# Kernel tuning notes

Hardware: AMD Instinct MI355X
Metric: run time of the kernel (lower is better)

## Reference

```python
import jax, jax.numpy as jnp
import numpy as np

N, E = 100000, 1600000
IN_C, H, C = 256, 4, 64
NEG_SLOPE = 0.2


def setup_inputs() -> dict:
    key = jax.random.key(0)
    k1, k2, k3, k4, k5 = jax.random.split(key, 5)
    x = jax.random.normal(k1, (N, IN_C), dtype=jnp.float32)
    edge_index = jax.random.randint(k2, (2, E), 0, N, dtype=jnp.int64)
    # GATConv params: lin weight [IN_C, H*C], attention vectors [H, C], bias [C] (concat=False)
    W = jax.random.normal(k3, (IN_C, H * C), dtype=jnp.float32) / np.sqrt(IN_C)
    att_src = jax.random.normal(k4, (H, C), dtype=jnp.float32) / np.sqrt(C)
    att_dst = jax.random.normal(k5, (H, C), dtype=jnp.float32) / np.sqrt(C)
    bias = jnp.zeros((C,), dtype=jnp.float32)
    return {"x": x, "edge_index": edge_index, "W": W,
            "att_src": att_src, "att_dst": att_dst, "bias": bias}


def reference(x, edge_index, W, att_src, att_dst, bias):
    n = x.shape[0]
    # GATConv adds self-loops by default
    loops = jnp.arange(n, dtype=edge_index.dtype)
    src = jnp.concatenate([edge_index[0], loops])  # message source j
    dst = jnp.concatenate([edge_index[1], loops])  # message target i

    h = (x @ W).reshape(n, H, C)                       # [N,H,C]
    a_src = jnp.einsum('nhc,hc->nh', h, att_src)       # [N,H]
    a_dst = jnp.einsum('nhc,hc->nh', h, att_dst)       # [N,H]

    e = jax.nn.leaky_relu(a_src[src] + a_dst[dst], NEG_SLOPE)  # [E+N,H]
    m = jax.ops.segment_max(e, dst, num_segments=n)            # per-target max
    e = jnp.exp(e - m[dst])
    denom = jax.ops.segment_sum(e, dst, num_segments=n)
    alpha = e / (denom[dst] + 1e-16)                           # softmax over incoming edges

    out = jax.ops.segment_sum(alpha[:, :, None] * h[src], dst, num_segments=n)  # [N,H,C]
    return out.mean(axis=1) + bias  # concat=False -> mean over heads, [N,C]
```

## Files before the change

kernel.cpp:

```cpp
#include <hip/hip_runtime.h>

#define N_NODES 100000
#define N_EDGES 1600000
#define TOT (N_EDGES + N_NODES)
#define IN_CH 256
#define NHEAD 4
#define CH 64
#define HC 256
#define NEG_SLOPE 0.2f
#define CAP 48
#define NGEMM ((N_NODES + 63) / 64)
#define DOTS_BLOCKS ((N_NODES + 3) / 4)
#define SCT_BLOCKS ((TOT + 255) / 256)

typedef _Float16 half8 __attribute__((ext_vector_type(8)));
typedef _Float16 h2v __attribute__((ext_vector_type(2)));
typedef float f32x4 __attribute__((ext_vector_type(4)));
typedef unsigned short ushort_t;
typedef unsigned int uint_t;

static __device__ __forceinline__ ushort_t f2h(float f) {
  _Float16 h = (_Float16)f;
  return __builtin_bit_cast(ushort_t, h);
}

static __device__ __forceinline__ void gload_lds16(const char* g, char* l) {
  __builtin_amdgcn_global_load_lds(
      (const __attribute__((address_space(1))) unsigned int*)g,
      (__attribute__((address_space(3))) unsigned int*)l, 16, 0, 0);
}

__global__ __launch_bounds__(256) void conv_w(const float* __restrict__ W,
                                              const float* __restrict__ att_src,
                                              const float* __restrict__ att_dst,
                                              uint4* __restrict__ Wt_arr,
                                              float4* __restrict__ Was4,
                                              float4* __restrict__ Wad4,
                                              int* __restrict__ cursor) {
  int id = blockIdx.x * 256 + threadIdx.x;
  if (blockIdx.x == 32) {
    int k = threadIdx.x;
    float s[4] = {}, d[4] = {};
#pragma unroll
    for (int h = 0; h < 4; ++h) {
      const float4* wr = reinterpret_cast<const float4*>(W + (size_t)k * HC + h * 64);
      const float4* asr = reinterpret_cast<const float4*>(att_src + h * 64);
      const float4* adr = reinterpret_cast<const float4*>(att_dst + h * 64);
      for (int c4 = 0; c4 < 16; ++c4) {
        float4 w = wr[c4], a = asr[c4], b = adr[c4];
        s[h] += w.x * a.x + w.y * a.y + w.z * a.z + w.w * a.w;
        d[h] += w.x * b.x + w.y * b.y + w.z * b.z + w.w * b.w;
      }
    }
    Was4[k] = make_float4(s[0], s[1], s[2], s[3]);
    Wad4[k] = make_float4(d[0], d[1], d[2], d[3]);
  } else {
    int lane = id & 63;
    int n = (id >> 6) & 15;
    int ks = id >> 10;
    int col = n * 16 + (lane & 15);
    int kbase = ks * 32 + (lane >> 4) * 8;
    ushort_t h[8];
#pragma unroll
    for (int j = 0; j < 8; ++j) h[j] = f2h(W[(size_t)(kbase + j) * HC + col]);
    uint4 u;
    u.x = (uint_t)h[0] | ((uint_t)h[1] << 16);
    u.y = (uint_t)h[2] | ((uint_t)h[3] << 16);
    u.z = (uint_t)h[4] | ((uint_t)h[5] << 16);
    u.w = (uint_t)h[6] | ((uint_t)h[7] << 16);
    Wt_arr[id] = u;
  }
  for (int i = id; i < N_NODES / 4; i += 33 * 256)
    reinterpret_cast<int4*>(cursor)[i] = make_int4(0, 0, 0, 0);
}

__global__ __launch_bounds__(256) void dots(const float* __restrict__ X,
                                            const float4* __restrict__ Was4,
                                            const float4* __restrict__ Wad4,
                                            float* __restrict__ as_buf,
                                            float* __restrict__ ad_buf) {
  int n = blockIdx.x * 4 + (threadIdx.x >> 6);
  int lane = threadIdx.x & 63;
  if (n >= N_NODES) return;
  float4 xv = reinterpret_cast<const float4*>(X)[(size_t)n * 64 + lane];
  const float4* ws = Was4 + lane * 4;
  const float4* wd = Wad4 + lane * 4;
  float s[4] = {}, d[4] = {};
  float xj[4] = {xv.x, xv.y, xv.z, xv.w};
#pragma unroll
  for (int j = 0; j < 4; ++j) {
    float4 a = ws[j], b = wd[j];
    s[0] += xj[j] * a.x; s[1] += xj[j] * a.y; s[2] += xj[j] * a.z; s[3] += xj[j] * a.w;
    d[0] += xj[j] * b.x; d[1] += xj[j] * b.y; d[2] += xj[j] * b.z; d[3] += xj[j] * b.w;
  }
#pragma unroll
  for (int off = 32; off > 0; off >>= 1) {
#pragma unroll
    for (int h = 0; h < 4; ++h) {
      s[h] += __shfl_xor(s[h], off, 64);
      d[h] += __shfl_xor(d[h], off, 64);
    }
  }
  if (lane == 0) {
    *reinterpret_cast<float4*>(as_buf + (size_t)n * 4) = make_float4(s[0], s[1], s[2], s[3]);
    *reinterpret_cast<float4*>(ad_buf + (size_t)n * 4) = make_float4(d[0], d[1], d[2], d[3]);
  }
}

__global__ __launch_bounds__(256) void scatter_gemm(const int* __restrict__ esrc,
                                                    const int* __restrict__ edst,
                                                    const float* __restrict__ as_buf,
                                                    const float* __restrict__ ad_buf,
                                                    int* __restrict__ cursor,
                                                    uint4* __restrict__ erec,
                                                    const float* __restrict__ X,
                                                    const uint4* __restrict__ Wt_arr,
                                                    uint2* __restrict__ Hmp, int M) {
  const int tid = threadIdx.x;

  if (blockIdx.x < SCT_BLOCKS) {
    int e = blockIdx.x * 256 + tid;
    if (e >= TOT) return;
    int s, d;
    if (e < N_EDGES) { s = esrc[e]; d = edst[e]; }
    else { s = e - N_EDGES; d = s; }
    int p = atomicAdd(&cursor[d], 1);
    if (p >= CAP) p = CAP - 1;
    float4 a1 = *reinterpret_cast<const float4*>(as_buf + (size_t)s * NHEAD);
    float4 a2 = *reinterpret_cast<const float4*>(ad_buf + (size_t)d * NHEAD);
    float e0 = a1.x + a2.x; e0 = e0 > 0.f ? e0 : NEG_SLOPE * e0;
    float e1 = a1.y + a2.y; e1 = e1 > 0.f ? e1 : NEG_SLOPE * e1;
    float e2 = a1.z + a2.z; e2 = e2 > 0.f ? e2 : NEG_SLOPE * e2;
    float e3 = a1.w + a2.w; e3 = e3 > 0.f ? e3 : NEG_SLOPE * e3;
    float w0 = __expf(e0 - 4.f), w1 = __expf(e1 - 4.f);
    float w2 = __expf(e2 - 4.f), w3 = __expf(e3 - 4.f);
    uint_t pk01 = __builtin_bit_cast(uint_t, __builtin_amdgcn_cvt_pkrtz(w0, w1));
    uint_t pk23 = __builtin_bit_cast(uint_t, __builtin_amdgcn_cvt_pkrtz(w2, w3));
    erec[(size_t)d * CAP + p] = make_uint4((uint_t)s, pk01, pk23, 0u);
    return;
  }

  __shared__ uint4 Bs[3][1024];
  __shared__ __align__(16) float As[3][2048];
  const int lane = tid & 63;
  const int wid = tid >> 6;
  const int l16 = lane & 15;
  const int lhi = lane >> 4;
  const int row0 = (blockIdx.x - SCT_BLOCKS) * 64;

  const int arow = tid >> 3;
  const int aslot = tid & 7;
  int ga0 = row0 + arow;       if (ga0 >= M) ga0 = M - 1;
  int ga1 = row0 + arow + 32;  if (ga1 >= M) ga1 = M - 1;
  const int sslot = aslot ^ (arow & 7);
  const char* asrc0 = (const char*)X + (size_t)ga0 * 1024 + (sslot << 4);
  const char* asrc1 = (const char*)X + (size_t)ga1 * 1024 + (sslot << 4);

  const char* __restrict__ wsrc = (const char*)Wt_arr;

  const int frow = wid * 16 + l16;
  const int sw = frow & 7;
  const int fo0 = frow * 32 + (((2 * lhi + 0) ^ sw) << 2);
  const int fo1 = frow * 32 + (((2 * lhi + 1) ^ sw) << 2);

  auto ISSUE = [&](int kk, int b) {
    char* ad = (char*)&As[b][0] + tid * 16;
    gload_lds16(asrc0 + kk * 128, ad);
    gload_lds16(asrc1 + kk * 128, ad + 4096);
    char* bd = (char*)&Bs[b][0] + tid * 16;
    const char* s = wsrc + kk * 16384 + tid * 16;
    gload_lds16(s,         bd);
    gload_lds16(s + 4096,  bd + 4096);
    gload_lds16(s + 8192,  bd + 8192);
    gload_lds16(s + 12288, bd + 12288);
  };

  ISSUE(0, 0);
  ISSUE(1, 1);

  f32x4 acc[16] = {};

#pragma unroll
  for (int ks = 0; ks < 8; ++ks) {
    __builtin_amdgcn_s_barrier();
    if (ks < 6) ISSUE(ks + 2, (ks + 2) % 3);
    if (ks < 6)       asm volatile("s_waitcnt vmcnt(12)" ::: "memory");
    else if (ks == 6) asm volatile("s_waitcnt vmcnt(6)" ::: "memory");
    else              asm volatile("s_waitcnt vmcnt(0)" ::: "memory");

    const float* Ab = &As[ks % 3][0];
    float4 f0 = *reinterpret_cast<const float4*>(Ab + fo0);
    float4 f1 = *reinterpret_cast<const float4*>(Ab + fo1);
    uint4 ua;
    ua.x = __builtin_bit_cast(uint_t, __builtin_amdgcn_cvt_pkrtz(f0.x, f0.y));
    ua.y = __builtin_bit_cast(uint_t, __builtin_amdgcn_cvt_pkrtz(f0.z, f0.w));
    ua.z = __builtin_bit_cast(uint_t, __builtin_amdgcn_cvt_pkrtz(f1.x, f1.y));
    ua.w = __builtin_bit_cast(uint_t, __builtin_amdgcn_cvt_pkrtz(f1.z, f1.w));
    half8 a = __builtin_bit_cast(half8, ua);

    const char* bbase = (const char*)&Bs[ks % 3][0];
#pragma unroll
    for (int n = 0; n < 16; ++n) {
      half8 b = *reinterpret_cast<const half8*>(bbase + n * 1024 + lane * 16);
      acc[n] = __builtin_amdgcn_mfma_f32_16x16x32_f16(a, b, acc[n], 0, 0, 0);
    }
  }

#pragma unroll
  for (int r = 0; r < 4; ++r) {
    int grow = row0 + wid * 16 + lhi * 4 + r;
    if (grow < M) {
#pragma unroll
      for (int n2 = 0; n2 < 4; ++n2) {
        uint_t pk01 = __builtin_bit_cast(uint_t,
            __builtin_amdgcn_cvt_pkrtz(acc[n2][r], acc[n2 + 4][r]));
        uint_t pk23 = __builtin_bit_cast(uint_t,
            __builtin_amdgcn_cvt_pkrtz(acc[n2 + 8][r], acc[n2 + 12][r]));
        Hmp[(size_t)grow * 64 + n2 * 16 + l16] = make_uint2(pk01, pk23);
      }
    }
  }
}

static __device__ __forceinline__ void accum_edge(uint4 cur, uint4 hv, bool act,
                                                  float* acc, float* den) {
  uint_t w01u = act ? cur.y : 0u;
  uint_t w23u = act ? cur.z : 0u;
  h2v w01 = __builtin_bit_cast(h2v, w01u);
  h2v w23 = __builtin_bit_cast(h2v, w23u);
  h2v ha = __builtin_bit_cast(h2v, hv.x);
  h2v hb = __builtin_bit_cast(h2v, hv.y);
  h2v hc = __builtin_bit_cast(h2v, hv.z);
  h2v hd = __builtin_bit_cast(h2v, hv.w);
  acc[0] += (float)w01.x * (float)ha.x;
  acc[1] += (float)w01.y * (float)ha.y;
  acc[2] += (float)w23.x * (float)hb.x;
  acc[3] += (float)w23.y * (float)hb.y;
  acc[4] += (float)w01.x * (float)hc.x;
  acc[5] += (float)w01.y * (float)hc.y;
  acc[6] += (float)w23.x * (float)hd.x;
  acc[7] += (float)w23.y * (float)hd.y;
  den[0] += (float)w01.x;
  den[1] += (float)w01.y;
  den[2] += (float)w23.x;
  den[3] += (float)w23.y;
}

__global__ __launch_bounds__(256) void aggregate(const int* __restrict__ cursor,
                                                 const uint4* __restrict__ erec,
                                                 const uint2* __restrict__ Hp,
                                                 const float* __restrict__ bias,
                                                 float* __restrict__ out) {
  int n = blockIdx.x * 4 + (threadIdx.x >> 6);
  int lane = threadIdx.x & 63;
  if (n >= N_NODES) return;
  const int half = lane >> 5;
  const uint_t off_lane = (uint_t)(lane & 31) << 4;
  const char* __restrict__ Hb = (const char*)Hp;

  int cnt = cursor[n];
  if (cnt > CAP) cnt = CAP;
  const int beg = n * CAP;
  const int end = beg + cnt;
  const int last = end - 1;

  float acc[8] = {};
  float den[4] = {};

  int i0 = beg + half;     if (i0 > last) i0 = last;
  int i1 = beg + 2 + half; if (i1 > last) i1 = last;
  int i2 = beg + 4 + half; if (i2 > last) i2 = last;
  int i3 = beg + 6 + half; if (i3 > last) i3 = last;
  uint4 r0 = erec[i0], r1 = erec[i1], r2 = erec[i2], r3 = erec[i3];

  for (int j = beg; j < end; j += 8) {
    uint4 c0 = r0, c1 = r1, c2 = r2, c3 = r3;
    i0 = j + 8 + half;  if (i0 > last) i0 = last;
    i1 = j + 10 + half; if (i1 > last) i1 = last;
    i2 = j + 12 + half; if (i2 > last) i2 = last;
    i3 = j + 14 + half; if (i3 > last) i3 = last;
    r0 = erec[i0]; r1 = erec[i1]; r2 = erec[i2]; r3 = erec[i3];

    uint4 h0 = *reinterpret_cast<const uint4*>(Hb + ((c0.x << 9) | off_lane));
    uint4 h1 = *reinterpret_cast<const uint4*>(Hb + ((c1.x << 9) | off_lane));
    uint4 h2 = *reinterpret_cast<const uint4*>(Hb + ((c2.x << 9) | off_lane));
    uint4 h3 = *reinterpret_cast<const uint4*>(Hb + ((c3.x << 9) | off_lane));

    accum_edge(c0, h0, (j + half) < end, acc, den);
    accum_edge(c1, h1, (j + 2 + half) < end, acc, den);
    accum_edge(c2, h2, (j + 4 + half) < end, acc, den);
    accum_edge(c3, h3, (j + 6 + half) < end, acc, den);
  }

#pragma unroll
  for (int k = 0; k < 8; ++k) acc[k] += __shfl_xor(acc[k], 32, 64);
#pragma unroll
  for (int k = 0; k < 4; ++k) den[k] += __shfl_xor(den[k], 32, 64);

  if (lane < 32) {
    float i0v = 1.f / (den[0] + 1e-30f);
    float i1v = 1.f / (den[1] + 1e-30f);
    float i2v = 1.f / (den[2] + 1e-30f);
    float i3v = 1.f / (den[3] + 1e-30f);
    float2 b2 = *reinterpret_cast<const float2*>(bias + 2 * lane);
    float rA = 0.25f * (acc[0] * i0v + acc[1] * i1v + acc[2] * i2v + acc[3] * i3v) + b2.x;
    float rB = 0.25f * (acc[4] * i0v + acc[5] * i1v + acc[6] * i2v + acc[7] * i3v) + b2.y;
    *reinterpret_cast<float2*>(out + (size_t)n * CH + 2 * lane) = make_float2(rA, rB);
  }
}

extern "C" void kernel_launch(void* const* d_in, const int* in_sizes, int n_in,
                              void* d_out, int out_size, void* d_ws, size_t ws_size,
                              hipStream_t stream) {
  const float* x       = (const float*)d_in[0];
  const int*   eidx    = (const int*)d_in[1];
  const float* W       = (const float*)d_in[2];
  const float* att_src = (const float*)d_in[3];
  const float* att_dst = (const float*)d_in[4];
  const float* bias    = (const float*)d_in[5];
  float* out = (float*)d_out;

  uint2*  Hmp    = (uint2*)d_ws;
  uint4*  erec   = (uint4*)(Hmp + (size_t)N_NODES * 64);
  float*  as_buf = (float*)(erec + (size_t)N_NODES * CAP);
  float*  ad_buf = as_buf + (size_t)N_NODES * NHEAD;
  uint4*  Wt_arr = (uint4*)(ad_buf + (size_t)N_NODES * NHEAD);
  float4* Was4   = (float4*)(Wt_arr + 8192);
  float4* Wad4   = Was4 + 256;
  int*    cursor = (int*)(Wad4 + 256);

  const int* esrc = eidx;
  const int* edst = eidx + N_EDGES;

  conv_w<<<33, 256, 0, stream>>>(W, att_src, att_dst, Wt_arr, Was4, Wad4, cursor);

  dots<<<DOTS_BLOCKS, 256, 0, stream>>>(x, Was4, Wad4, as_buf, ad_buf);

  scatter_gemm<<<SCT_BLOCKS + NGEMM, 256, 0, stream>>>(esrc, edst, as_buf, ad_buf,
                                                       cursor, erec, x, Wt_arr,
                                                       Hmp, N_NODES);

  aggregate<<<(N_NODES + 3) / 4, 256, 0, stream>>>(cursor, erec, Hmp, bias, out);
}
```

Baseline: 288.5 us.

## Write self-loop edge records in dots kernel and use nontemporal edge-record access

Self-loop edge records are now written directly by the dots kernel into slot 0 of each node's bucket, and the cursor is initialised to 1 so the scatter only handles real edges, with no atomics needed for self-loops. Edge-record stores and loads become nontemporal so the scattered record traffic is less likely to evict the H feature rows, which aggregation gathers and reuses. The cost is extra per-node work in dots, plus a possible loss of cache reuse if the nontemporal hints misbehave.

```diff
diff --git a/kernel.cpp b/kernel.cpp
--- a/kernel.cpp
+++ b/kernel.cpp
@@ -2,7 +2,6 @@
 
 #define N_NODES 100000
 #define N_EDGES 1600000
-#define TOT (N_EDGES + N_NODES)
 #define IN_CH 256
 #define NHEAD 4
 #define CH 64
@@ -11,11 +10,12 @@
 #define CAP 48
 #define NGEMM ((N_NODES + 63) / 64)
 #define DOTS_BLOCKS ((N_NODES + 3) / 4)
-#define SCT_BLOCKS ((TOT + 255) / 256)
+#define SCT_BLOCKS ((N_EDGES + 255) / 256)
 
 typedef _Float16 half8 __attribute__((ext_vector_type(8)));
 typedef _Float16 h2v __attribute__((ext_vector_type(2)));
 typedef float f32x4 __attribute__((ext_vector_type(4)));
+typedef unsigned int u32x4 __attribute__((ext_vector_type(4)));
 typedef unsigned short ushort_t;
 typedef unsigned int uint_t;
 
@@ -28,6 +28,15 @@
   __builtin_amdgcn_global_load_lds(
       (const __attribute__((address_space(1))) unsigned int*)g,
       (__attribute__((address_space(3))) unsigned int*)l, 16, 0, 0);
+}
+
+static __device__ __forceinline__ void nt_store4(uint_t* p, uint_t a, uint_t b,
+                                                 uint_t c, uint_t d) {
+  u32x4 v = {a, b, c, d};
+  __builtin_nontemporal_store(v, reinterpret_cast<u32x4*>(p));
+}
+static __device__ __forceinline__ u32x4 nt_load4(const uint_t* p) {
+  return __builtin_nontemporal_load(reinterpret_cast<const u32x4*>(p));
 }
 
 __global__ __launch_bounds__(256) void conv_w(const float* __restrict__ W,
@@ -71,14 +80,15 @@
     Wt_arr[id] = u;
   }
   for (int i = id; i < N_NODES / 4; i += 33 * 256)
-    reinterpret_cast<int4*>(cursor)[i] = make_int4(0, 0, 0, 0);
+    reinterpret_cast<int4*>(cursor)[i] = make_int4(1, 1, 1, 1);
 }
 
 __global__ __launch_bounds__(256) void dots(const float* __restrict__ X,
                                             const float4* __restrict__ Was4,
                                             const float4* __restrict__ Wad4,
                                             float* __restrict__ as_buf,
-                                            float* __restrict__ ad_buf) {
+                                            float* __restrict__ ad_buf,
+                                            uint_t* __restrict__ erec) {
   int n = blockIdx.x * 4 + (threadIdx.x >> 6);
   int lane = threadIdx.x & 63;
   if (n >= N_NODES) return;
@@ -104,6 +114,15 @@
   if (lane == 0) {
     *reinterpret_cast<float4*>(as_buf + (size_t)n * 4) = make_float4(s[0], s[1], s[2], s[3]);
     *reinterpret_cast<float4*>(ad_buf + (size_t)n * 4) = make_float4(d[0], d[1], d[2], d[3]);
+    float e0 = s[0] + d[0]; e0 = e0 > 0.f ? e0 : NEG_SLOPE * e0;
+    float e1 = s[1] + d[1]; e1 = e1 > 0.f ? e1 : NEG_SLOPE * e1;
+    float e2 = s[2] + d[2]; e2 = e2 > 0.f ? e2 : NEG_SLOPE * e2;
+    float e3 = s[3] + d[3]; e3 = e3 > 0.f ? e3 : NEG_SLOPE * e3;
+    float w0 = __expf(e0 - 4.f), w1 = __expf(e1 - 4.f);
+    float w2 = __expf(e2 - 4.f), w3 = __expf(e3 - 4.f);
+    uint_t pk01 = __builtin_bit_cast(uint_t, __builtin_amdgcn_cvt_pkrtz(w0, w1));
+    uint_t pk23 = __builtin_bit_cast(uint_t, __builtin_amdgcn_cvt_pkrtz(w2, w3));
+    nt_store4(erec + (size_t)n * CAP * 4, (uint_t)n, pk01, pk23, 0u);
   }
 }
 
@@ -112,7 +131,7 @@
                                                     const float* __restrict__ as_buf,
                                                     const float* __restrict__ ad_buf,
                                                     int* __restrict__ cursor,
-                                                    uint4* __restrict__ erec,
+                                                    uint_t* __restrict__ erec,
                                                     const float* __restrict__ X,
                                                     const uint4* __restrict__ Wt_arr,
                                                     uint2* __restrict__ Hmp, int M) {
@@ -120,10 +139,9 @@
 
   if (blockIdx.x < SCT_BLOCKS) {
     int e = blockIdx.x * 256 + tid;
-    if (e >= TOT) return;
-    int s, d;
-    if (e < N_EDGES) { s = esrc[e]; d = edst[e]; }
-    else { s = e - N_EDGES; d = s; }
+    if (e >= N_EDGES) return;
+    int s = esrc[e];
+    int d = edst[e];
     int p = atomicAdd(&cursor[d], 1);
     if (p >= CAP) p = CAP - 1;
     float4 a1 = *reinterpret_cast<const float4*>(as_buf + (size_t)s * NHEAD);
@@ -136,7 +154,7 @@
     float w2 = __expf(e2 - 4.f), w3 = __expf(e3 - 4.f);
     uint_t pk01 = __builtin_bit_cast(uint_t, __builtin_amdgcn_cvt_pkrtz(w0, w1));
     uint_t pk23 = __builtin_bit_cast(uint_t, __builtin_amdgcn_cvt_pkrtz(w2, w3));
-    erec[(size_t)d * CAP + p] = make_uint4((uint_t)s, pk01, pk23, 0u);
+    nt_store4(erec + ((size_t)d * CAP + p) * 4, (uint_t)s, pk01, pk23, 0u);
     return;
   }
 
@@ -222,7 +240,7 @@
   }
 }
 
-static __device__ __forceinline__ void accum_edge(uint4 cur, uint4 hv, bool act,
+static __device__ __forceinline__ void accum_edge(u32x4 cur, uint4 hv, bool act,
                                                   float* acc, float* den) {
   uint_t w01u = act ? cur.y : 0u;
   uint_t w23u = act ? cur.z : 0u;
@@ -247,7 +265,7 @@
 }
 
 __global__ __launch_bounds__(256) void aggregate(const int* __restrict__ cursor,
-                                                 const uint4* __restrict__ erec,
+                                                 const uint_t* __restrict__ erec,
                                                  const uint2* __restrict__ Hp,
                                                  const float* __restrict__ bias,
                                                  float* __restrict__ out) {
@@ -271,20 +289,26 @@
   int i1 = beg + 2 + half; if (i1 > last) i1 = last;
   int i2 = beg + 4 + half; if (i2 > last) i2 = last;
   int i3 = beg + 6 + half; if (i3 > last) i3 = last;
-  uint4 r0 = erec[i0], r1 = erec[i1], r2 = erec[i2], r3 = erec[i3];
+  u32x4 r0 = nt_load4(erec + (size_t)i0 * 4);
+  u32x4 r1 = nt_load4(erec + (size_t)i1 * 4);
+  u32x4 r2 = nt_load4(erec + (size_t)i2 * 4);
+  u32x4 r3 = nt_load4(erec + (size_t)i3 * 4);
 
   for (int j = beg; j < end; j += 8) {
-    uint4 c0 = r0, c1 = r1, c2 = r2, c3 = r3;
+    u32x4 c0 = r0, c1 = r1, c2 = r2, c3 = r3;
     i0 = j + 8 + half;  if (i0 > last) i0 = last;
     i1 = j + 10 + half; if (i1 > last) i1 = last;
     i2 = j + 12 + half; if (i2 > last) i2 = last;
     i3 = j + 14 + half; if (i3 > last) i3 = last;
-    r0 = erec[i0]; r1 = erec[i1]; r2 = erec[i2]; r3 = erec[i3];
-
-    uint4 h0 = *reinterpret_cast<const uint4*>(Hb + ((c0.x << 9) | off_lane));
-    uint4 h1 = *reinterpret_cast<const uint4*>(Hb + ((c1.x << 9) | off_lane));
-    uint4 h2 = *reinterpret_cast<const uint4*>(Hb + ((c2.x << 9) | off_lane));
-    uint4 h3 = *reinterpret_cast<const uint4*>(Hb + ((c3.x << 9) | off_lane));
+    r0 = nt_load4(erec + (size_t)i0 * 4);
+    r1 = nt_load4(erec + (size_t)i1 * 4);
+    r2 = nt_load4(erec + (size_t)i2 * 4);
+    r3 = nt_load4(erec + (size_t)i3 * 4);
+
+    uint4 h0 = *reinterpret_cast<const uint4*>(Hb + (((uint_t)c0.x << 9) | off_lane));
+    uint4 h1 = *reinterpret_cast<const uint4*>(Hb + (((uint_t)c1.x << 9) | off_lane));
+    uint4 h2 = *reinterpret_cast<const uint4*>(Hb + (((uint_t)c2.x << 9) | off_lane));
+    uint4 h3 = *reinterpret_cast<const uint4*>(Hb + (((uint_t)c3.x << 9) | off_lane));
 
     accum_edge(c0, h0, (j + half) < end, acc, den);
     accum_edge(c1, h1, (j + 2 + half) < end, acc, den);
@@ -321,8 +345,8 @@
   float* out = (float*)d_out;
 
   uint2*  Hmp    = (uint2*)d_ws;
-  uint4*  erec   = (uint4*)(Hmp + (size_t)N_NODES * 64);
-  float*  as_buf = (float*)(erec + (size_t)N_NODES * CAP);
+  uint_t* erec   = (uint_t*)(Hmp + (size_t)N_NODES * 64);
+  float*  as_buf = (float*)(erec + (size_t)N_NODES * CAP * 4);
   float*  ad_buf = as_buf + (size_t)N_NODES * NHEAD;
   uint4*  Wt_arr = (uint4*)(ad_buf + (size_t)N_NODES * NHEAD);
   float4* Was4   = (float4*)(Wt_arr + 8192);
@@ -334,7 +358,7 @@
 
   conv_w<<<33, 256, 0, stream>>>(W, att_src, att_dst, Wt_arr, Was4, Wad4, cursor);
 
-  dots<<<DOTS_BLOCKS, 256, 0, stream>>>(x, Was4, Wad4, as_buf, ad_buf);
+  dots<<<DOTS_BLOCKS, 256, 0, stream>>>(x, Was4, Wad4, as_buf, ad_buf, erec);
 
   scatter_gemm<<<SCT_BLOCKS + NGEMM, 256, 0, stream>>>(esrc, edst, as_buf, ad_buf,
                                                        cursor, erec, x, Wt_arr,
```

Result: slower. 306.7 us (+6.3%).
